# Optimization experiments

Hardware: AMD Instinct MI355X
Metric: run time of the kernel (lower is better)

Reference implementation:

```python
import jax, jax.numpy as jnp
import numpy as np

B, S, D = 2, 2048, 4096
N_HEADS, N_KV_HEADS, HEAD_DIM = 32, 8, 128
Q_DIM = N_HEADS * HEAD_DIM        # 4096
KV_DIM = N_KV_HEADS * HEAD_DIM    # 1024
N_REP = N_HEADS // N_KV_HEADS
ROPE_THETA = 500000.0


def make_freqs_cis(seqlen, head_dim, theta):
    # Interleaved (sin, cos) pairs per rotary frequency, matching the module's
    # einsum/flip RoPE convention: row1 = x0*sin + x1*cos, row0 = x0*cos - x1*sin.
    inv_freq = 1.0 / (theta ** (np.arange(0, head_dim, 2, dtype=np.float32) / head_dim))
    t = np.arange(seqlen, dtype=np.float32)
    ang = np.outer(t, inv_freq)                       # [S, hd/2]
    fc = np.stack([np.sin(ang), np.cos(ang)], axis=-1)  # [S, hd/2, 2]
    return jnp.asarray(fc.reshape(seqlen, head_dim))


def apply_rotary_emb(xq, xk, freqs_cis):
    # xq: [B,S,Hq,hd], xk: [B,S,Hkv,hd], freqs_cis: [S,hd]
    xq_shape, xk_shape = xq.shape, xk.shape
    xq2 = xq.reshape(*xq.shape[:-1], -1, 2)
    xk2 = xk.reshape(*xk.shape[:-1], -1, 2)
    fc = freqs_cis.reshape(freqs_cis.shape[0], 1, -1, 2)   # [S,1,hd/2,2]
    # row_1 = <x, fc>
    xq_row1 = jnp.einsum('bshpi,shpi->bshp', xq2, fc)
    xk_row1 = jnp.einsum('bshpi,shpi->bshp', xk2, fc)
    # flipped fc with negated second component: (f1, -f0)
    fc_flip = jnp.flip(fc, axis=-1) * jnp.array([1.0, -1.0], dtype=fc.dtype)
    xq_row0 = jnp.einsum('bshpi,shpi->bshp', xq2, fc_flip)
    xk_row0 = jnp.einsum('bshpi,shpi->bshp', xk2, fc_flip)
    xq_out = jnp.stack([xq_row0, xq_row1], axis=-1).reshape(xq_shape)
    xk_out = jnp.stack([xk_row0, xk_row1], axis=-1).reshape(xk_shape)
    return xq_out, xk_out


def setup_inputs() -> dict:
    key = jax.random.key(0)
    k1, k2, k3 = jax.random.split(key, 3)
    x = jax.random.normal(k1, (B, S, D), dtype=jnp.float32)
    wqkv = jax.random.normal(k2, (D, Q_DIM + 2 * KV_DIM), dtype=jnp.float32) * 0.02
    wo = jax.random.normal(k3, (Q_DIM, D), dtype=jnp.float32) * 0.02
    freqs_cis = make_freqs_cis(S, HEAD_DIM, ROPE_THETA)
    return {"x": x, "freqs_cis": freqs_cis, "wqkv": wqkv, "wo": wo, "is_causal": 1}


def reference(x, freqs_cis, wqkv, wo, is_causal):
    bsz, seqlen, _ = x.shape
    xqkv = jnp.einsum('bsd,de->bse', x, wqkv)
    xq = xqkv[..., :Q_DIM].reshape(bsz, seqlen, N_HEADS, HEAD_DIM)
    xk = xqkv[..., Q_DIM:Q_DIM + KV_DIM].reshape(bsz, seqlen, N_KV_HEADS, HEAD_DIM)
    xv = xqkv[..., Q_DIM + KV_DIM:].reshape(bsz, seqlen, N_KV_HEADS, HEAD_DIM)
    xq, xk = apply_rotary_emb(xq, xk, freqs_cis)
    # [B,H,S,hd]
    xq = xq.transpose(0, 2, 1, 3)
    xk = jnp.repeat(xk.transpose(0, 2, 1, 3), N_REP, axis=1)
    xv = jnp.repeat(xv.transpose(0, 2, 1, 3), N_REP, axis=1)
    scale = 1.0 / jnp.sqrt(jnp.asarray(HEAD_DIM, dtype=xq.dtype))
    scores = jnp.einsum('bhqd,bhkd->bhqk', xq, xk) * scale
    if is_causal:
        mask = jnp.tril(jnp.ones((seqlen, seqlen), dtype=bool))
        scores = jnp.where(mask, scores, jnp.finfo(scores.dtype).min)
    attn = jax.nn.softmax(scores, axis=-1)
    out = jnp.einsum('bhqk,bhkd->bhqd', attn, xv)
    out = out.transpose(0, 2, 1, 3).reshape(bsz, seqlen, Q_DIM)
    return jnp.einsum('bsd,de->bse', out, wo)
```

## Files before the change

kernel.cpp:

```cpp
#include <hip/hip_runtime.h>
#include <stdint.h>
#include <stddef.h>

#define BB 2
#define SS 2048
#define DD 4096
#define NH 32
#define NKV 8
#define HD 128
#define QDIM 4096
#define KVDIM 1024
#define NQKV 6144
#define NTILES 64
#define QK_SCALE_L2E 0.12751744f

typedef __bf16 bf16;
typedef __bf16 bf16x8 __attribute__((ext_vector_type(8)));
typedef __bf16 bf16x4 __attribute__((ext_vector_type(4)));
typedef float f32x4 __attribute__((ext_vector_type(4)));

#define MFMA16(a, b, c) __builtin_amdgcn_mfma_f32_16x16x32_bf16((a), (b), (c), 0, 0, 0)
#define VMW5() asm volatile("s_waitcnt vmcnt(5)" ::: "memory")
#define VMW4() asm volatile("s_waitcnt vmcnt(4)" ::: "memory")
#define VMW2() asm volatile("s_waitcnt vmcnt(2)" ::: "memory")
#define VMW0() asm volatile("s_waitcnt vmcnt(0)" ::: "memory")
#define BARX()                                  \
    do {                                        \
        __builtin_amdgcn_s_barrier();           \
        __builtin_amdgcn_sched_barrier(0);      \
    } while (0)
#define LGKM0_SGB()                                         \
    do {                                                    \
        asm volatile("s_waitcnt lgkmcnt(0)" ::: "memory");  \
        __builtin_amdgcn_sched_barrier(0);                  \
    } while (0)

typedef __attribute__((address_space(1))) void GASV;
typedef __attribute__((address_space(3))) void LASV;

__device__ __forceinline__ void gload_lds16(const void* g, void* l) {
    __builtin_amdgcn_global_load_lds((GASV*)g, (LASV*)l, 16, 0, 0);
}

__device__ __forceinline__ float fexp2(float x) {
    float r;
    asm("v_exp_f32 %0, %1" : "=v"(r) : "v"(x));
    return r;
}

__global__ __launch_bounds__(256) void k_cvt_x(const float* __restrict__ in,
                                               bf16* __restrict__ out) {
    size_t i = ((size_t)blockIdx.x * 256 + threadIdx.x) * 8;
    const float4 a = *(const float4*)(in + i);
    const float4 b = *(const float4*)(in + i + 4);
    bf16x8 v;
    v[0] = (bf16)a.x; v[1] = (bf16)a.y; v[2] = (bf16)a.z; v[3] = (bf16)a.w;
    v[4] = (bf16)b.x; v[5] = (bf16)b.y; v[6] = (bf16)b.z; v[7] = (bf16)b.w;
    *(bf16x8*)(out + i) = v;
}

__global__ __launch_bounds__(256) void k_tr_cvt(const float* __restrict__ in,
                                                bf16* __restrict__ out, int R, int C) {
    __shared__ float tile[64][65];
    const int t = threadIdx.x;
    const int tx = t & 15, ty = t >> 4;
    const int r0 = blockIdx.y * 64, c0 = blockIdx.x * 64;
#pragma unroll
    for (int p = 0; p < 4; ++p) {
        const float4 v = *(const float4*)(in + (size_t)(r0 + p * 16 + ty) * C + c0 + tx * 4);
        tile[p * 16 + ty][tx * 4 + 0] = v.x;
        tile[p * 16 + ty][tx * 4 + 1] = v.y;
        tile[p * 16 + ty][tx * 4 + 2] = v.z;
        tile[p * 16 + ty][tx * 4 + 3] = v.w;
    }
    __syncthreads();
#pragma unroll
    for (int p = 0; p < 4; ++p) {
        const int oc = c0 + p * 16 + ty;
        bf16x4 pk;
#pragma unroll
        for (int j = 0; j < 4; ++j) pk[j] = (bf16)tile[tx * 4 + j][p * 16 + ty];
        *(bf16x4*)(out + (size_t)oc * R + r0 + tx * 4) = pk;
    }
}

__device__ __forceinline__ void stage_half(char* ldsRegion, const bf16* gsrc) {
    const int t = threadIdx.x;
    const int wid = t >> 6;
#pragma unroll
    for (int i = 0; i < 2; ++i) {
        const int off = i * 8192 + t * 16;
        const int row = off >> 7;
        const int pc = (off >> 4) & 7;
        const int lc = pc ^ (row & 7);
        gload_lds16(gsrc + (size_t)row * 4096 + lc * 8,
                    ldsRegion + i * 8192 + wid * 1024);
    }
}

__device__ __forceinline__ void gemm256(const bf16* __restrict__ At,
                                        const bf16* __restrict__ Bt,
                                        char* LB, f32x4 acc[8][4]) {
    const int tid = threadIdx.x, lane = tid & 63, wid = tid >> 6;
    const int wm = wid >> 2, wn = wid & 3;
    const int l15 = lane & 15, l4 = lane >> 4;

    const f32x4 vz = {0.f, 0.f, 0.f, 0.f};
#pragma unroll
    for (int m = 0; m < 8; ++m)
#pragma unroll
        for (int n = 0; n < 4; ++n) acc[m][n] = vz;

    auto Areg = [&](int db, int h) -> char* { return LB + db * 32768 + h * 16384; };
    auto Breg = [&](int db, int h) -> char* { return LB + 65536 + db * 32768 + h * 16384; };

    bf16x8 RA[2][4], RAb[2][4], RB0[2][2], RB1[2][2];

    auto loadA = [&](bf16x8 dst[2][4], int db, int h) {
        char* base = Areg(db, h);
#pragma unroll
        for (int kk = 0; kk < 2; ++kk)
#pragma unroll
            for (int mf = 0; mf < 4; ++mf) {
                const int row = wm * 64 + mf * 16 + l15;
                const int cc = kk * 4 + l4;
                dst[kk][mf] = *(const bf16x8*)(base + row * 128 + ((cc ^ (row & 7)) << 4));
            }
    };
    auto loadB = [&](bf16x8 dst[2][2], int db, int h) {
        char* base = Breg(db, h);
#pragma unroll
        for (int kk = 0; kk < 2; ++kk)
#pragma unroll
            for (int nf = 0; nf < 2; ++nf) {
                const int row = wn * 32 + nf * 16 + l15;
                const int cc = kk * 4 + l4;
                dst[kk][nf] = *(const bf16x8*)(base + row * 128 + ((cc ^ (row & 7)) << 4));
            }
    };
    auto stA = [&](int tau, int h) {
        stage_half(Areg(tau & 1, h), At + (size_t)(h * 128) * 4096 + tau * 64);
    };
    auto stB = [&](int tau, int h) {
        stage_half(Breg(tau & 1, h), Bt + (size_t)(h * 128) * 4096 + tau * 64);
    };
    auto mma = [&](bf16x8 A[2][4], bf16x8 B[2][2], int mb, int nb) {
        __builtin_amdgcn_s_setprio(1);
#pragma unroll
        for (int kk = 0; kk < 2; ++kk)
#pragma unroll
            for (int mf = 0; mf < 4; ++mf)
#pragma unroll
                for (int nf = 0; nf < 2; ++nf)
                    acc[mb + mf][nb + nf] = MFMA16(A[kk][mf], B[kk][nf], acc[mb + mf][nb + nf]);
        __builtin_amdgcn_s_setprio(0);
    };

    stA(0, 0); stB(0, 0);
    stB(0, 1); stA(0, 1);
    VMW4();
    BARX();

#pragma unroll 1
    for (int tau = 0; tau < NTILES - 1; ++tau) {
        const int db = tau & 1;
        loadA(RA, db, 0);
        loadB(RB0, db, 0);
        stA(tau + 1, 0);
        stB(tau + 1, 0);
        VMW4();
        BARX(); LGKM0_SGB();
        mma(RA, RB0, 0, 0);
        BARX();
        loadB(RB1, db, 1);
        stB(tau + 1, 1);
        stA(tau + 1, 1);
        BARX(); LGKM0_SGB();
        mma(RA, RB1, 0, 2);
        BARX();
        loadA(RAb, db, 1);
        VMW4();
        BARX(); LGKM0_SGB();
        mma(RAb, RB0, 4, 0);
        mma(RAb, RB1, 4, 2);
        BARX();
    }

    VMW0();
    BARX();
    {
        const int db = (NTILES - 1) & 1;
        loadA(RA, db, 0);
        loadB(RB0, db, 0);
        mma(RA, RB0, 0, 0);
        loadB(RB1, db, 1);
        mma(RA, RB1, 0, 2);
        loadA(RAb, db, 1);
        mma(RAb, RB0, 4, 0);
        mma(RAb, RB1, 4, 2);
    }
}

__device__ __forceinline__ void stage_B192(char* ldsRegion, const bf16* gsrc) {
    const int t = threadIdx.x;
    const int wid = t >> 6;
#pragma unroll
    for (int i = 0; i < 3; ++i) {
        const int off = i * 8192 + t * 16;
        const int row = off >> 7;
        const int pc = (off >> 4) & 7;
        const int lc = pc ^ (row & 7);
        gload_lds16(gsrc + (size_t)row * 4096 + lc * 8,
                    ldsRegion + i * 8192 + wid * 1024);
    }
}

__device__ __forceinline__ void gemm192(const bf16* __restrict__ At,
                                        const bf16* __restrict__ Bt,
                                        char* LB, f32x4 acc[8][3]) {
    const int tid = threadIdx.x, lane = tid & 63, wid = tid >> 6;
    const int wm = wid >> 2, wn = wid & 3;
    const int l15 = lane & 15, l4 = lane >> 4;

    const f32x4 vz = {0.f, 0.f, 0.f, 0.f};
#pragma unroll
    for (int m = 0; m < 8; ++m)
#pragma unroll
        for (int n = 0; n < 3; ++n) acc[m][n] = vz;

    auto Areg = [&](int db, int h) -> char* { return LB + db * 32768 + h * 16384; };
    auto Breg = [&](int db) -> char* { return LB + 65536 + db * 24576; };

    bf16x8 RA[2][4], RAb[2][4], RB0[2][2], RB1[2];

    auto loadA = [&](bf16x8 dst[2][4], int db, int h) {
        char* base = Areg(db, h);
#pragma unroll
        for (int kk = 0; kk < 2; ++kk)
#pragma unroll
            for (int mf = 0; mf < 4; ++mf) {
                const int row = wm * 64 + mf * 16 + l15;
                const int cc = kk * 4 + l4;
                dst[kk][mf] = *(const bf16x8*)(base + row * 128 + ((cc ^ (row & 7)) << 4));
            }
    };
    auto loadB0 = [&](int db) {
        char* base = Breg(db);
#pragma unroll
        for (int kk = 0; kk < 2; ++kk)
#pragma unroll
            for (int nf = 0; nf < 2; ++nf) {
                const int row = wn * 48 + nf * 16 + l15;
                const int cc = kk * 4 + l4;
                RB0[kk][nf] = *(const bf16x8*)(base + row * 128 + ((cc ^ (row & 7)) << 4));
            }
    };
    auto loadB1 = [&](int db) {
        char* base = Breg(db);
#pragma unroll
        for (int kk = 0; kk < 2; ++kk) {
            const int row = wn * 48 + 32 + l15;
            const int cc = kk * 4 + l4;
            RB1[kk] = *(const bf16x8*)(base + row * 128 + ((cc ^ (row & 7)) << 4));
        }
    };
    auto stA = [&](int tau, int h) {
        stage_half(Areg(tau & 1, h), At + (size_t)(h * 128) * 4096 + tau * 64);
    };
    auto stB = [&](int tau) {
        stage_B192(Breg(tau & 1), Bt + tau * 64);
    };
    auto mmaB0 = [&](bf16x8 A[2][4], int mb) {
        __builtin_amdgcn_s_setprio(1);
#pragma unroll
        for (int kk = 0; kk < 2; ++kk)
#pragma unroll
            for (int mf = 0; mf < 4; ++mf)
#pragma unroll
                for (int nf = 0; nf < 2; ++nf)
                    acc[mb + mf][nf] = MFMA16(A[kk][mf], RB0[kk][nf], acc[mb + mf][nf]);
        __builtin_amdgcn_s_setprio(0);
    };
    auto mmaB1 = [&](bf16x8 A[2][4], int mb) {
        __builtin_amdgcn_s_setprio(1);
#pragma unroll
        for (int kk = 0; kk < 2; ++kk)
#pragma unroll
            for (int mf = 0; mf < 4; ++mf)
                acc[mb + mf][2] = MFMA16(A[kk][mf], RB1[kk], acc[mb + mf][2]);
        __builtin_amdgcn_s_setprio(0);
    };

    stA(0, 0); stB(0);
    stA(0, 1);
    VMW2();
    BARX();

#pragma unroll 1
    for (int tau = 0; tau < NTILES - 1; ++tau) {
        const int db = tau & 1;
        loadA(RA, db, 0);
        loadB0(db);
        stA(tau + 1, 0);
        stB(tau + 1);
        VMW5();
        BARX(); LGKM0_SGB();
        mmaB0(RA, 0);
        BARX();
        loadB1(db);
        stA(tau + 1, 1);
        BARX(); LGKM0_SGB();
        mmaB1(RA, 0);
        BARX();
        loadA(RAb, db, 1);
        VMW2();
        BARX(); LGKM0_SGB();
        mmaB0(RAb, 4);
        mmaB1(RAb, 4);
        BARX();
    }

    VMW0();
    BARX();
    {
        const int db = (NTILES - 1) & 1;
        loadA(RA, db, 0);
        loadB0(db);
        mmaB0(RA, 0);
        loadB1(db);
        mmaB1(RA, 0);
        loadA(RAb, db, 1);
        mmaB0(RAb, 4);
        mmaB1(RAb, 4);
    }
}

__device__ __forceinline__ void xcd_swizzle(int gx, int& bx, int& by) {
    const int nwg = gx * gridDim.y;
    int lin = by * gx + bx;
    lin = (lin & 7) * (nwg >> 3) + (lin >> 3);
    bx = lin % gx;
    by = lin / gx;
}

__global__ __launch_bounds__(512, 2) void k_gemm_qkv(const bf16* __restrict__ A,
                                                     const bf16* __restrict__ Bt,
                                                     const float* __restrict__ fc,
                                                     bf16* __restrict__ Qb,
                                                     bf16* __restrict__ Kb,
                                                     bf16* __restrict__ VTb) {
    __shared__ __align__(16) char LB[114688];
    f32x4 acc[8][3];
    int bx = blockIdx.x, by = blockIdx.y;
    xcd_swizzle(NQKV / 192, bx, by);
    gemm192(A + (size_t)by * 256 * 4096, Bt + (size_t)bx * 192 * 4096, LB, acc);

    const int tid = threadIdx.x, lane = tid & 63, wid = tid >> 6;
    const int wm = wid >> 2, wn = wid & 3;
    const int l15 = lane & 15, l4 = lane >> 4;
#pragma unroll
    for (int mf = 0; mf < 8; ++mf) {
        const int rowbase = by * 256 + (mf >> 2) * 128 + wm * 64 + (mf & 3) * 16 + l4 * 4;
#pragma unroll
        for (int nf = 0; nf < 3; ++nf) {
            const int rb = bx * 192 + wn * 48 + nf * 16;
            const int col = rb + l15;
            f32x4 v = acc[mf][nf];
            if (rb < QDIM + KVDIM) {
                const int d = col & (HD - 1);
                const int dp = d & ~1;
                const float sgn = (d & 1) ? 1.f : -1.f;
#pragma unroll
                for (int r = 0; r < 4; ++r) {
                    const int row = rowbase + r;
                    const int s = row & (SS - 1);
                    const float2 sc = *(const float2*)(fc + s * HD + dp);
                    const float partner = __shfl_xor(v[r], 1);
                    float res = v[r] * sc.y + sgn * partner * sc.x;
                    if (rb < QDIM) {
                        res *= QK_SCALE_L2E;
                        Qb[(size_t)row * QDIM + col] = (bf16)res;
                    } else {
                        Kb[(size_t)row * KVDIM + (col - QDIM)] = (bf16)res;
                    }
                }
            } else {
                const int hdv = col - (QDIM + KVDIM);
                const int kvh = hdv >> 7, dd = hdv & (HD - 1);
                const int bb = rowbase >> 11, s = rowbase & (SS - 1);
                bf16x4 pk;
#pragma unroll
                for (int r = 0; r < 4; ++r) pk[r] = (bf16)v[r];
                *(bf16x4*)(VTb + ((size_t)((bb * NKV + kvh) * HD + dd)) * SS + s) = pk;
            }
        }
    }
}

__global__ __launch_bounds__(512, 2) void k_gemm_out(const bf16* __restrict__ A,
                                                     const bf16* __restrict__ Bt,
                                                     float* __restrict__ out) {
    __shared__ __align__(16) char LB[131072];
    f32x4 acc[8][4];
    int bx = blockIdx.x, by = blockIdx.y;
    xcd_swizzle(DD / 256, bx, by);
    gemm256(A + (size_t)by * 256 * 4096, Bt + (size_t)bx * 256 * 4096, LB, acc);

    const int tid = threadIdx.x, lane = tid & 63, wid = tid >> 6;
    const int wm = wid >> 2, wn = wid & 3;
    const int l15 = lane & 15, l4 = lane >> 4;
#pragma unroll
    for (int mf = 0; mf < 8; ++mf) {
        const int row = by * 256 + (mf >> 2) * 128 + wm * 64 + (mf & 3) * 16 + l4 * 4;
#pragma unroll
        for (int nf = 0; nf < 4; ++nf) {
            const int col = bx * 256 + (nf >> 1) * 128 + wn * 32 + (nf & 1) * 16 + l15;
#pragma unroll
            for (int r = 0; r < 4; ++r) out[(size_t)(row + r) * DD + col] = acc[mf][nf][r];
        }
    }
}

__global__ __launch_bounds__(256, 2) void k_attn(const bf16* __restrict__ Qb,
                                                 const bf16* __restrict__ Kb,
                                                 const bf16* __restrict__ VTb,
                                                 bf16* __restrict__ Ob) {
    __shared__ __align__(16) bf16 Ks[64 * 128];
    __shared__ __align__(16) bf16 Vs[128 * 64];
    __shared__ __align__(16) bf16 Ps[4][32 * 88];
    int lin = (blockIdx.z * NH + blockIdx.y) * 8 + blockIdx.x;
    lin = (lin & 7) * 64 + (lin >> 3);
    const int jj = lin & 7, h = (lin >> 3) & (NH - 1), b = lin >> 8;
    const int kvh = h >> 2;
    const int tid = threadIdx.x, lane = tid & 63, w = tid >> 6;
    const int l15 = lane & 15, l4 = lane >> 4;

    const bf16* Kg = Kb + (size_t)b * SS * KVDIM + kvh * HD;
    const bf16* Vg = VTb + (size_t)(b * NKV + kvh) * HD * SS;

    int4 kreg[4], vreg[4];
    const f32x4 vz = {0.f, 0.f, 0.f, 0.f};

    auto issue_kv = [&](int t) {
#pragma unroll
        for (int i = 0; i < 4; ++i) {
            const int off = i * 4096 + tid * 16;
            const int row = off >> 8;
            const int cc = (off >> 4) & 15;
            kreg[i] = *(const int4*)((const char*)(Kg + (size_t)(t * 64 + row) * KVDIM) + cc * 16);
        }
#pragma unroll
        for (int i = 0; i < 4; ++i) {
            const int off = i * 4096 + tid * 16;
            const int row = off >> 7;
            const int cc = (off >> 4) & 7;
            vreg[i] = *(const int4*)((const char*)(Vg + (size_t)row * SS + t * 64) + cc * 16);
        }
    };

#pragma unroll 1
    for (int pj = 0; pj < 2; ++pj) {
        const int j = pj ? (15 - jj) : jj;
        const int q0 = j * 128;
        const int nt = 2 * j + 2;

        bf16x8 qf[2][4];
#pragma unroll
        for (int m = 0; m < 2; ++m) {
            const int qrow = q0 + w * 32 + m * 16 + l15;
            const bf16* qb = Qb + ((size_t)(b * SS + qrow) << 12) + h * HD + l4 * 8;
#pragma unroll
            for (int kc = 0; kc < 4; ++kc) qf[m][kc] = *(const bf16x8*)(qb + kc * 32);
        }

        f32x4 o[2][8];
#pragma unroll
        for (int m = 0; m < 2; ++m)
#pragma unroll
            for (int df = 0; df < 8; ++df) o[m][df] = vz;
        float m_run[2][4], l_run[2][4];
#pragma unroll
        for (int m = 0; m < 2; ++m)
#pragma unroll
            for (int r = 0; r < 4; ++r) { m_run[m][r] = -1e30f; l_run[m][r] = 0.f; }

        issue_kv(0);

        for (int t = 0; t < nt; ++t) {
            __syncthreads();
#pragma unroll
            for (int i = 0; i < 4; ++i) {
                const int off = i * 4096 + tid * 16;
                const int row = off >> 8;
                const int cc = (off >> 4) & 15;
                const int lc = cc ^ (row & 7);
                *(int4*)((char*)Ks + row * 256 + lc * 16) = kreg[i];
            }
#pragma unroll
            for (int i = 0; i < 4; ++i) {
                const int off = i * 4096 + tid * 16;
                const int row = off >> 7;
                const int cc = (off >> 4) & 7;
                const int lc = cc ^ (row & 7);
                *(int4*)((char*)Vs + row * 128 + lc * 16) = vreg[i];
            }
            __syncthreads();

            if (t + 1 < nt) issue_kv(t + 1);

            f32x4 sa[2][4];
#pragma unroll
            for (int m = 0; m < 2; ++m)
#pragma unroll
                for (int n = 0; n < 4; ++n) sa[m][n] = vz;
            __builtin_amdgcn_s_setprio(1);
#pragma unroll
            for (int kc = 0; kc < 4; ++kc)
#pragma unroll
                for (int n = 0; n < 4; ++n) {
                    const int krow = n * 16 + l15;
                    const int cc = kc * 4 + l4;
                    const bf16x8 kf =
                        *(const bf16x8*)((const char*)Ks + (krow << 8) + ((cc ^ (krow & 7)) << 4));
                    sa[0][n] = MFMA16(qf[0][kc], kf, sa[0][n]);
                    sa[1][n] = MFMA16(qf[1][kc], kf, sa[1][n]);
                }
            __builtin_amdgcn_s_setprio(0);

            if (t >= 2 * j) {
#pragma unroll
                for (int m = 0; m < 2; ++m)
#pragma unroll
                    for (int n = 0; n < 4; ++n)
#pragma unroll
                        for (int r = 0; r < 4; ++r) {
                            const int col = t * 64 + n * 16 + l15;
                            const int qr = q0 + w * 32 + m * 16 + l4 * 4 + r;
                            if (col > qr) sa[m][n][r] = -1e30f;
                        }
            }

#pragma unroll
            for (int m = 0; m < 2; ++m)
#pragma unroll
                for (int r = 0; r < 4; ++r) {
                    float mx = fmaxf(fmaxf(sa[m][0][r], sa[m][1][r]),
                                     fmaxf(sa[m][2][r], sa[m][3][r]));
#pragma unroll
                    for (int mk = 1; mk <= 8; mk <<= 1) mx = fmaxf(mx, __shfl_xor(mx, mk));
                    const float mn = fmaxf(m_run[m][r], mx);
                    const float alpha = fexp2(m_run[m][r] - mn);
                    m_run[m][r] = mn;
                    float rs = 0.f;
#pragma unroll
                    for (int n = 0; n < 4; ++n) {
                        const float p = fexp2(sa[m][n][r] - mn);
                        sa[m][n][r] = p;
                        rs += p;
                    }
#pragma unroll
                    for (int mk = 1; mk <= 8; mk <<= 1) rs += __shfl_xor(rs, mk);
                    l_run[m][r] = l_run[m][r] * alpha + rs;
#pragma unroll
                    for (int df = 0; df < 8; ++df) o[m][df][r] *= alpha;
                }

#pragma unroll
            for (int m = 0; m < 2; ++m)
#pragma unroll
                for (int n = 0; n < 4; ++n)
#pragma unroll
                    for (int r = 0; r < 4; ++r)
                        Ps[w][(m * 16 + l4 * 4 + r) * 88 + n * 16 + l15] = (bf16)sa[m][n][r];

            bf16x8 pf0[2], pf1[2];
#pragma unroll
            for (int ks = 0; ks < 2; ++ks) {
                pf0[ks] = *(const bf16x8*)(&Ps[w][l15 * 88 + ks * 32 + l4 * 8]);
                pf1[ks] = *(const bf16x8*)(&Ps[w][(16 + l15) * 88 + ks * 32 + l4 * 8]);
            }

            __builtin_amdgcn_s_setprio(1);
#pragma unroll
            for (int df = 0; df < 8; ++df)
#pragma unroll
                for (int ks = 0; ks < 2; ++ks) {
                    const int vrow = df * 16 + l15;
                    const int cc = ks * 4 + l4;
                    const bf16x8 vf =
                        *(const bf16x8*)((const char*)Vs + (vrow << 7) + ((cc ^ (vrow & 7)) << 4));
                    o[0][df] = MFMA16(pf0[ks], vf, o[0][df]);
                    o[1][df] = MFMA16(pf1[ks], vf, o[1][df]);
                }
            __builtin_amdgcn_s_setprio(0);
        }

#pragma unroll
        for (int m = 0; m < 2; ++m)
#pragma unroll
            for (int r = 0; r < 4; ++r) {
                const float inv = 1.f / l_run[m][r];
                const size_t row = (size_t)(b * SS + q0 + w * 32 + m * 16 + l4 * 4 + r);
#pragma unroll
                for (int df = 0; df < 8; ++df)
                    Ob[(row << 12) + h * HD + df * 16 + l15] = (bf16)(o[m][df][r] * inv);
            }
    }
}

extern "C" void kernel_launch(void* const* d_in, const int* in_sizes, int n_in,
                              void* d_out, int out_size, void* d_ws, size_t ws_size,
                              hipStream_t stream) {
    const float* x    = (const float*)d_in[0];
    const float* fc   = (const float*)d_in[1];
    const float* wqkv = (const float*)d_in[2];
    const float* wo   = (const float*)d_in[3];

    char* wsp = (char*)d_ws;
    const size_t MB = (size_t)1 << 20;
    bf16* xb    = (bf16*)(wsp);
    bf16* wqkvT = (bf16*)(wsp + 32 * MB);
    bf16* woT   = (bf16*)(wsp + 32 * MB);
    bf16* Qb    = (bf16*)(wsp + 80 * MB);
    bf16* Kb    = (bf16*)(wsp + 112 * MB);
    bf16* VTb   = (bf16*)(wsp + 120 * MB);
    bf16* Ab    = (bf16*)(wsp);
    float* out  = (float*)d_out;

    k_cvt_x<<<8192, 256, 0, stream>>>(x, xb);
    k_tr_cvt<<<dim3(NQKV / 64, DD / 64), 256, 0, stream>>>(wqkv, wqkvT, DD, NQKV);
    k_gemm_qkv<<<dim3(NQKV / 192, (BB * SS) / 256), 512, 0, stream>>>(xb, wqkvT, fc, Qb, Kb, VTb);
    k_tr_cvt<<<dim3(DD / 64, QDIM / 64), 256, 0, stream>>>(wo, woT, QDIM, DD);
    k_attn<<<dim3(8, NH, BB), 256, 0, stream>>>(Qb, Kb, VTb, Ab);
    k_gemm_out<<<dim3(DD / 256, (BB * SS) / 256), 512, 0, stream>>>(Ab, woT, out);
}
```

Baseline: 569.5 us.

## Stage 128-key KV tiles in attention and widen transpose-convert output stores

The attention kernel now stages 128 keys of K and V per barrier pair instead of 64 and processes each tile as two 64-key halves, so the number of block-wide syncs per query block is halved. The K/V LDS buffers grow to 32 KB each with a 16-way XOR swizzle, and the P scratch buffer becomes unpadded with an XOR swizzle. The weight transpose-convert kernel handles 128 rows per block and writes 8-wide bf16 vectors. The larger LDS footprint and doubled prefetch registers per thread may reduce occupancy under the two-block launch bound.

```diff
diff --git a/kernel.cpp b/kernel.cpp
--- a/kernel.cpp
+++ b/kernel.cpp
@@ -61,12 +61,12 @@
 
 __global__ __launch_bounds__(256) void k_tr_cvt(const float* __restrict__ in,
                                                 bf16* __restrict__ out, int R, int C) {
-    __shared__ float tile[64][65];
+    __shared__ float tile[128][65];
     const int t = threadIdx.x;
     const int tx = t & 15, ty = t >> 4;
-    const int r0 = blockIdx.y * 64, c0 = blockIdx.x * 64;
-#pragma unroll
-    for (int p = 0; p < 4; ++p) {
+    const int r0 = blockIdx.y * 128, c0 = blockIdx.x * 64;
+#pragma unroll
+    for (int p = 0; p < 8; ++p) {
         const float4 v = *(const float4*)(in + (size_t)(r0 + p * 16 + ty) * C + c0 + tx * 4);
         tile[p * 16 + ty][tx * 4 + 0] = v.x;
         tile[p * 16 + ty][tx * 4 + 1] = v.y;
@@ -75,12 +75,12 @@
     }
     __syncthreads();
 #pragma unroll
-    for (int p = 0; p < 4; ++p) {
-        const int oc = c0 + p * 16 + ty;
-        bf16x4 pk;
-#pragma unroll
-        for (int j = 0; j < 4; ++j) pk[j] = (bf16)tile[tx * 4 + j][p * 16 + ty];
-        *(bf16x4*)(out + (size_t)oc * R + r0 + tx * 4) = pk;
+    for (int q = 0; q < 4; ++q) {
+        const int lc = q * 16 + ty;
+        bf16x8 pk;
+#pragma unroll
+        for (int jx = 0; jx < 8; ++jx) pk[jx] = (bf16)tile[tx * 8 + jx][lc];
+        *(bf16x8*)(out + (size_t)(c0 + lc) * R + r0 + tx * 8) = pk;
     }
 }
 
@@ -425,9 +425,9 @@
                                                  const bf16* __restrict__ Kb,
                                                  const bf16* __restrict__ VTb,
                                                  bf16* __restrict__ Ob) {
-    __shared__ __align__(16) bf16 Ks[64 * 128];
-    __shared__ __align__(16) bf16 Vs[128 * 64];
-    __shared__ __align__(16) bf16 Ps[4][32 * 88];
+    __shared__ __align__(16) char Ks[32768];
+    __shared__ __align__(16) char Vs[32768];
+    __shared__ __align__(16) bf16 Ps[4][32 * 64];
     int lin = (blockIdx.z * NH + blockIdx.y) * 8 + blockIdx.x;
     lin = (lin & 7) * 64 + (lin >> 3);
     const int jj = lin & 7, h = (lin >> 3) & (NH - 1), b = lin >> 8;
@@ -438,23 +438,23 @@
     const bf16* Kg = Kb + (size_t)b * SS * KVDIM + kvh * HD;
     const bf16* Vg = VTb + (size_t)(b * NKV + kvh) * HD * SS;
 
-    int4 kreg[4], vreg[4];
+    int4 kreg[8], vreg[8];
     const f32x4 vz = {0.f, 0.f, 0.f, 0.f};
 
-    auto issue_kv = [&](int t) {
-#pragma unroll
-        for (int i = 0; i < 4; ++i) {
+    auto issue_kv = [&](int T) {
+#pragma unroll
+        for (int i = 0; i < 8; ++i) {
             const int off = i * 4096 + tid * 16;
             const int row = off >> 8;
             const int cc = (off >> 4) & 15;
-            kreg[i] = *(const int4*)((const char*)(Kg + (size_t)(t * 64 + row) * KVDIM) + cc * 16);
+            kreg[i] = *(const int4*)((const char*)(Kg + (size_t)(T * 128 + row) * KVDIM) + cc * 16);
         }
 #pragma unroll
-        for (int i = 0; i < 4; ++i) {
+        for (int i = 0; i < 8; ++i) {
             const int off = i * 4096 + tid * 16;
-            const int row = off >> 7;
-            const int cc = (off >> 4) & 7;
-            vreg[i] = *(const int4*)((const char*)(Vg + (size_t)row * SS + t * 64) + cc * 16);
+            const int row = off >> 8;
+            const int cc = (off >> 4) & 15;
+            vreg[i] = *(const int4*)((const char*)(Vg + (size_t)row * SS + T * 128) + cc * 16);
         }
     };
 
@@ -462,7 +462,7 @@
     for (int pj = 0; pj < 2; ++pj) {
         const int j = pj ? (15 - jj) : jj;
         const int q0 = j * 128;
-        const int nt = 2 * j + 2;
+        const int nT = j + 1;
 
         bf16x8 qf[2][4];
 #pragma unroll
@@ -486,113 +486,120 @@
 
         issue_kv(0);
 
-        for (int t = 0; t < nt; ++t) {
+        for (int T = 0; T < nT; ++T) {
             __syncthreads();
 #pragma unroll
-            for (int i = 0; i < 4; ++i) {
+            for (int i = 0; i < 8; ++i) {
                 const int off = i * 4096 + tid * 16;
                 const int row = off >> 8;
-                const int cc = (off >> 4) & 15;
-                const int lc = cc ^ (row & 7);
-                *(int4*)((char*)Ks + row * 256 + lc * 16) = kreg[i];
-            }
-#pragma unroll
-            for (int i = 0; i < 4; ++i) {
+                const int lc = ((off >> 4) & 15) ^ (row & 15);
+                *(int4*)(Ks + row * 256 + lc * 16) = kreg[i];
+            }
+#pragma unroll
+            for (int i = 0; i < 8; ++i) {
                 const int off = i * 4096 + tid * 16;
-                const int row = off >> 7;
-                const int cc = (off >> 4) & 7;
-                const int lc = cc ^ (row & 7);
-                *(int4*)((char*)Vs + row * 128 + lc * 16) = vreg[i];
+                const int row = off >> 8;
+                const int lc = ((off >> 4) & 15) ^ (row & 15);
+                *(int4*)(Vs + row * 256 + lc * 16) = vreg[i];
             }
             __syncthreads();
 
-            if (t + 1 < nt) issue_kv(t + 1);
-
-            f32x4 sa[2][4];
-#pragma unroll
-            for (int m = 0; m < 2; ++m)
-#pragma unroll
-                for (int n = 0; n < 4; ++n) sa[m][n] = vz;
-            __builtin_amdgcn_s_setprio(1);
-#pragma unroll
-            for (int kc = 0; kc < 4; ++kc)
-#pragma unroll
-                for (int n = 0; n < 4; ++n) {
-                    const int krow = n * 16 + l15;
-                    const int cc = kc * 4 + l4;
-                    const bf16x8 kf =
-                        *(const bf16x8*)((const char*)Ks + (krow << 8) + ((cc ^ (krow & 7)) << 4));
-                    sa[0][n] = MFMA16(qf[0][kc], kf, sa[0][n]);
-                    sa[1][n] = MFMA16(qf[1][kc], kf, sa[1][n]);
+            if (T + 1 < nT) issue_kv(T + 1);
+
+#pragma unroll
+            for (int hh = 0; hh < 2; ++hh) {
+                const int t = 2 * T + hh;
+
+                f32x4 sa[2][4];
+#pragma unroll
+                for (int m = 0; m < 2; ++m)
+#pragma unroll
+                    for (int n = 0; n < 4; ++n) sa[m][n] = vz;
+                __builtin_amdgcn_s_setprio(1);
+#pragma unroll
+                for (int kc = 0; kc < 4; ++kc)
+#pragma unroll
+                    for (int n = 0; n < 4; ++n) {
+                        const int krow = hh * 64 + n * 16 + l15;
+                        const bf16x8 kf = *(const bf16x8*)(
+                            Ks + krow * 256 + (((kc * 4 + l4) ^ (krow & 15)) << 4));
+                        sa[0][n] = MFMA16(qf[0][kc], kf, sa[0][n]);
+                        sa[1][n] = MFMA16(qf[1][kc], kf, sa[1][n]);
+                    }
+                __builtin_amdgcn_s_setprio(0);
+
+                if (t >= 2 * j) {
+#pragma unroll
+                    for (int m = 0; m < 2; ++m)
+#pragma unroll
+                        for (int n = 0; n < 4; ++n)
+#pragma unroll
+                            for (int r = 0; r < 4; ++r) {
+                                const int col = t * 64 + n * 16 + l15;
+                                const int qr = q0 + w * 32 + m * 16 + l4 * 4 + r;
+                                if (col > qr) sa[m][n][r] = -1e30f;
+                            }
                 }
-            __builtin_amdgcn_s_setprio(0);
-
-            if (t >= 2 * j) {
+
 #pragma unroll
                 for (int m = 0; m < 2; ++m)
 #pragma unroll
+                    for (int r = 0; r < 4; ++r) {
+                        float mx = fmaxf(fmaxf(sa[m][0][r], sa[m][1][r]),
+                                         fmaxf(sa[m][2][r], sa[m][3][r]));
+#pragma unroll
+                        for (int mk = 1; mk <= 8; mk <<= 1) mx = fmaxf(mx, __shfl_xor(mx, mk));
+                        const float mn = fmaxf(m_run[m][r], mx);
+                        const float alpha = fexp2(m_run[m][r] - mn);
+                        m_run[m][r] = mn;
+                        float rs = 0.f;
+#pragma unroll
+                        for (int n = 0; n < 4; ++n) {
+                            const float p = fexp2(sa[m][n][r] - mn);
+                            sa[m][n][r] = p;
+                            rs += p;
+                        }
+#pragma unroll
+                        for (int mk = 1; mk <= 8; mk <<= 1) rs += __shfl_xor(rs, mk);
+                        l_run[m][r] = l_run[m][r] * alpha + rs;
+#pragma unroll
+                        for (int df = 0; df < 8; ++df) o[m][df][r] *= alpha;
+                    }
+
+#pragma unroll
+                for (int m = 0; m < 2; ++m)
+#pragma unroll
                     for (int n = 0; n < 4; ++n)
 #pragma unroll
                         for (int r = 0; r < 4; ++r) {
-                            const int col = t * 64 + n * 16 + l15;
-                            const int qr = q0 + w * 32 + m * 16 + l4 * 4 + r;
-                            if (col > qr) sa[m][n][r] = -1e30f;
+                            const int prow = m * 16 + l4 * 4 + r;
+                            const int col = n * 16 + l15;
+                            const int pcol = (((col >> 3) ^ (prow & 7)) << 3) + (col & 7);
+                            Ps[w][prow * 64 + pcol] = (bf16)sa[m][n][r];
                         }
-            }
-
-#pragma unroll
-            for (int m = 0; m < 2; ++m)
-#pragma unroll
-                for (int r = 0; r < 4; ++r) {
-                    float mx = fmaxf(fmaxf(sa[m][0][r], sa[m][1][r]),
-                                     fmaxf(sa[m][2][r], sa[m][3][r]));
-#pragma unroll
-                    for (int mk = 1; mk <= 8; mk <<= 1) mx = fmaxf(mx, __shfl_xor(mx, mk));
-                    const float mn = fmaxf(m_run[m][r], mx);
-                    const float alpha = fexp2(m_run[m][r] - mn);
-                    m_run[m][r] = mn;
-                    float rs = 0.f;
-#pragma unroll
-                    for (int n = 0; n < 4; ++n) {
-                        const float p = fexp2(sa[m][n][r] - mn);
-                        sa[m][n][r] = p;
-                        rs += p;
+
+                bf16x8 pf0[2], pf1[2];
+#pragma unroll
+                for (int ks = 0; ks < 2; ++ks) {
+                    pf0[ks] = *(const bf16x8*)(
+                        &Ps[w][l15 * 64 + (((ks * 4 + l4) ^ (l15 & 7)) << 3)]);
+                    pf1[ks] = *(const bf16x8*)(
+                        &Ps[w][(16 + l15) * 64 + (((ks * 4 + l4) ^ (l15 & 7)) << 3)]);
+                }
+
+                __builtin_amdgcn_s_setprio(1);
+#pragma unroll
+                for (int df = 0; df < 8; ++df)
+#pragma unroll
+                    for (int ks = 0; ks < 2; ++ks) {
+                        const int vrow = df * 16 + l15;
+                        const bf16x8 vf = *(const bf16x8*)(
+                            Vs + vrow * 256 + (((hh * 8 + ks * 4 + l4) ^ (vrow & 15)) << 4));
+                        o[0][df] = MFMA16(pf0[ks], vf, o[0][df]);
+                        o[1][df] = MFMA16(pf1[ks], vf, o[1][df]);
                     }
-#pragma unroll
-                    for (int mk = 1; mk <= 8; mk <<= 1) rs += __shfl_xor(rs, mk);
-                    l_run[m][r] = l_run[m][r] * alpha + rs;
-#pragma unroll
-                    for (int df = 0; df < 8; ++df) o[m][df][r] *= alpha;
-                }
-
-#pragma unroll
-            for (int m = 0; m < 2; ++m)
-#pragma unroll
-                for (int n = 0; n < 4; ++n)
-#pragma unroll
-                    for (int r = 0; r < 4; ++r)
-                        Ps[w][(m * 16 + l4 * 4 + r) * 88 + n * 16 + l15] = (bf16)sa[m][n][r];
-
-            bf16x8 pf0[2], pf1[2];
-#pragma unroll
-            for (int ks = 0; ks < 2; ++ks) {
-                pf0[ks] = *(const bf16x8*)(&Ps[w][l15 * 88 + ks * 32 + l4 * 8]);
-                pf1[ks] = *(const bf16x8*)(&Ps[w][(16 + l15) * 88 + ks * 32 + l4 * 8]);
-            }
-
-            __builtin_amdgcn_s_setprio(1);
-#pragma unroll
-            for (int df = 0; df < 8; ++df)
-#pragma unroll
-                for (int ks = 0; ks < 2; ++ks) {
-                    const int vrow = df * 16 + l15;
-                    const int cc = ks * 4 + l4;
-                    const bf16x8 vf =
-                        *(const bf16x8*)((const char*)Vs + (vrow << 7) + ((cc ^ (vrow & 7)) << 4));
-                    o[0][df] = MFMA16(pf0[ks], vf, o[0][df]);
-                    o[1][df] = MFMA16(pf1[ks], vf, o[1][df]);
-                }
-            __builtin_amdgcn_s_setprio(0);
+                __builtin_amdgcn_s_setprio(0);
+            }
         }
 
 #pragma unroll
@@ -628,9 +635,9 @@
     float* out  = (float*)d_out;
 
     k_cvt_x<<<8192, 256, 0, stream>>>(x, xb);
-    k_tr_cvt<<<dim3(NQKV / 64, DD / 64), 256, 0, stream>>>(wqkv, wqkvT, DD, NQKV);
+    k_tr_cvt<<<dim3(NQKV / 64, DD / 128), 256, 0, stream>>>(wqkv, wqkvT, DD, NQKV);
     k_gemm_qkv<<<dim3(NQKV / 192, (BB * SS) / 256), 512, 0, stream>>>(xb, wqkvT, fc, Qb, Kb, VTb);
-    k_tr_cvt<<<dim3(DD / 64, QDIM / 64), 256, 0, stream>>>(wo, woT, QDIM, DD);
+    k_tr_cvt<<<dim3(DD / 64, QDIM / 128), 256, 0, stream>>>(wo, woT, QDIM, DD);
     k_attn<<<dim3(8, NH, BB), 256, 0, stream>>>(Qb, Kb, VTb, Ab);
     k_gemm_out<<<dim3(DD / 256, (BB * SS) / 256), 512, 0, stream>>>(Ab, woT, out);
 }
```

New measurement: 870.4 us. +52.8%, slower.
